# Performance work log

Measured on AMD Instinct MI355X. Metric: run time of the kernel, lower is better.

The kernel has to match this reference:

```python
import jax, jax.numpy as jnp
import numpy as np

B, D, L, K = 4096, 2048, 16384, 64  # batch, input_dim, latent_dim, topk


def setup_inputs() -> dict:
    key = jax.random.key(0)
    k_x, k_w = jax.random.split(key, 2)
    x = jax.random.normal(k_x, (B, D), dtype=jnp.float32)
    # torch init: randn(input_dim, latent_dim) / sqrt(input_dim)
    W_enc = jax.random.normal(k_w, (D, L), dtype=jnp.float32) / np.float32(np.sqrt(D))
    b_enc = jnp.zeros((L,), dtype=jnp.float32)
    b_dec = jnp.zeros((D,), dtype=jnp.float32)
    return {"x": x, "W_enc": W_enc, "b_enc": b_enc, "b_dec": b_dec, "k": K}


def reference(x, W_enc, b_enc, b_dec, k):
    # encode: [B, D] @ [D, L] + [L]
    z = x @ W_enc + b_enc
    # topk sparsify on |z| (do_abs_topk=True): scatter a 0/1 mask, multiply
    _, idx = jax.lax.top_k(jnp.abs(z), k)                      # idx: [B, k]
    rows = jnp.arange(z.shape[0])[:, None]                     # [B, 1]
    mask = jnp.zeros_like(z).at[rows, idx].set(1.0)            # [B, L]
    z_sparse = z * mask
    # decode with tied weights: [B, L] @ [L, D] + [D]
    recon = z_sparse @ W_enc.T + b_dec
    return recon, z_sparse
```

## Files before the change

### kernel.cpp

```cpp
#include <hip/hip_runtime.h>
#include <stdint.h>

#define NB 4096
#define DD 2048
#define LL 16384
#define KT 64
#define WCAP 24
#define TAU 1.2e-2f

typedef unsigned short u16;
typedef __bf16 bf16x8 __attribute__((ext_vector_type(8)));
typedef float f32x4 __attribute__((ext_vector_type(4)));
typedef unsigned short u16x4 __attribute__((ext_vector_type(4)));
typedef unsigned short u16x8 __attribute__((ext_vector_type(8)));

__device__ __forceinline__ float bf2f(u16 b) {
  return __uint_as_float(((unsigned)b) << 16);
}
__device__ __forceinline__ u16 f2bf(float f) {
  unsigned u = __float_as_uint(f);
  unsigned r = u + 0x7fffu + ((u >> 16) & 1u);
  return (u16)(r >> 16);
}

__global__ __launch_bounds__(256) void prep_x(const float* __restrict__ X,
                                              u16* __restrict__ Xh) {
  int i = (blockIdx.x * 256 + threadIdx.x) * 4;
  float4 v = *(const float4*)(X + i);
  u16x4 h;
  h[0] = f2bf(v.x); h[1] = f2bf(v.y); h[2] = f2bf(v.z); h[3] = f2bf(v.w);
  *(u16x4*)(Xh + i) = h;
}

__global__ __launch_bounds__(256) void prep_w(const float* __restrict__ W,
                                              u16* __restrict__ Wh,
                                              float* __restrict__ Wt) {
  __shared__ float tile[64][65];
  int l0 = blockIdx.x * 64, d0 = blockIdx.y * 64;
  int t = threadIdx.x;
  int lx = (t & 15) * 4;
  int dq = t >> 4;
#pragma unroll
  for (int p = 0; p < 4; ++p) {
    int d = dq + p * 16;
    float4 v = *(const float4*)(W + (size_t)(d0 + d) * LL + l0 + lx);
    tile[d][lx + 0] = v.x; tile[d][lx + 1] = v.y;
    tile[d][lx + 2] = v.z; tile[d][lx + 3] = v.w;
  }
  __syncthreads();
  int dx = (t & 15) * 4;
  int lq = t >> 4;
#pragma unroll
  for (int p = 0; p < 4; ++p) {
    int l = lq + p * 16;
    u16x4 h;
    float4 wv;
#pragma unroll
    for (int q = 0; q < 4; ++q) {
      float w = tile[dx + q][l];
      h[q] = f2bf(w);
      ((float*)&wv)[q] = w;
    }
    size_t o = (size_t)(l0 + l) * DD + d0 + dx;
    *(u16x4*)(Wh + o) = h;
    *(float4*)(Wt + o) = wv;
  }
}

#define TBM 256
#define TBN 256
#define TBK 64
#define NKT (DD / TBK)

__device__ __forceinline__ void async16(const u16* g, u16* l) {
  __builtin_amdgcn_global_load_lds(
      (const __attribute__((address_space(1))) unsigned int*)g,
      (__attribute__((address_space(3))) unsigned int*)l, 16, 0, 0);
}

#define STAGE(HF, TAU_)                                                      \
  do {                                                                       \
    const u16* g_ = ((HF) < 2 ? Abase : Bbase) +                             \
                    (size_t)(((HF)&1) * 128 + rr) * DD + ((TAU_) << 6) +     \
                    scol;                                                    \
    u16* l_ = ((HF) < 2 ? As : Bs) + ((TAU_)&1) * (TBM * TBK) +              \
              (((HF)&1) * 128) * TBK + t * 8;                                \
    async16(g_, l_);                                                         \
    async16(g_ + (size_t)64 * DD, l_ + 4096);                                \
  } while (0)

#define LDA(DST, DB, MQ)                                                     \
  do {                                                                       \
    const u16* p_ = As + (DB) * (TBM * TBK) + (wm + (MQ)*64 + fr) * TBK;     \
    _Pragma("unroll") for (int i_ = 0; i_ < 4; ++i_) {                       \
      DST[i_][0] = *(const bf16x8*)(p_ + i_ * (16 * TBK) + c0);              \
      DST[i_][1] = *(const bf16x8*)(p_ + i_ * (16 * TBK) + c1);              \
    }                                                                        \
  } while (0)

#define LDBQ(DB, NQ)                                                         \
  do {                                                                       \
    const u16* p_ = Bs + (DB) * (TBN * TBK) + (wn + (NQ)*32 + fr) * TBK;     \
    _Pragma("unroll") for (int j_ = 0; j_ < 2; ++j_) {                       \
      bq[j_][0] = *(const bf16x8*)(p_ + j_ * (16 * TBK) + c0);               \
      bq[j_][1] = *(const bf16x8*)(p_ + j_ * (16 * TBK) + c1);               \
    }                                                                        \
  } while (0)

#define MFMAQ(AF, MQ, NQ)                                                    \
  do {                                                                       \
    _Pragma("unroll") for (int i_ = 0; i_ < 4; ++i_)                         \
        _Pragma("unroll") for (int j_ = 0; j_ < 2; ++j_) {                   \
      f32x4 a_ = acc[(MQ)*4 + i_][(NQ)*2 + j_];                              \
      a_ = __builtin_amdgcn_mfma_f32_16x16x32_bf16(AF[i_][0], bq[j_][0], a_, \
                                                   0, 0, 0);                 \
      a_ = __builtin_amdgcn_mfma_f32_16x16x32_bf16(AF[i_][1], bq[j_][1], a_, \
                                                   0, 0, 0);                 \
      acc[(MQ)*4 + i_][(NQ)*2 + j_] = a_;                                    \
    }                                                                        \
  } while (0)

#define BAR __builtin_amdgcn_s_barrier()
#define LGKM0 asm volatile("s_waitcnt lgkmcnt(0)")
#define LGKM8 asm volatile("s_waitcnt lgkmcnt(8)")
#define PRIO1 __builtin_amdgcn_s_setprio(1)
#define PRIO0 __builtin_amdgcn_s_setprio(0)

__global__ __launch_bounds__(512, 2) void encode_gemm(
    const u16* __restrict__ Xh,
    const u16* __restrict__ Wh,
    const float* __restrict__ benc,
    float* __restrict__ Z) {
  __shared__ u16 As[2 * TBM * TBK];
  __shared__ u16 Bs[2 * TBN * TBK];
  int t = threadIdx.x;
  int m0 = blockIdx.y * TBM;
  int n0 = blockIdx.x * TBN;

  int lane = t & 63, w = t >> 6;
  int wm = (w & 1) * 128;
  int wn = (w >> 1) * 64;
  int fr = lane & 15;
  int fq = lane >> 4;
  int c0 = ((fq ^ (fr & 7)) << 3);
  int c1 = (((4 + fq) ^ (fr & 7)) << 3);
  int rr = t >> 3;
  int scol = (((t & 7) ^ (rr & 7)) << 3);

  const u16* Abase = Xh + (size_t)m0 * DD;
  const u16* Bbase = Wh + (size_t)n0 * DD;

  f32x4 acc[8][4] = {};
  bf16x8 af0[4][2], af1[4][2], bq[2][2];

  STAGE(0, 0); STAGE(1, 0); STAGE(2, 0); STAGE(3, 0);
  asm volatile("s_waitcnt vmcnt(4)" ::: "memory");
  STAGE(0, 1); STAGE(1, 1); STAGE(2, 1);
  asm volatile("s_waitcnt vmcnt(6)" ::: "memory");
  BAR;

  for (int it = 0; it < NKT / 2; ++it) {
    const int notlast = (it < NKT / 2 - 1);
    LDA(af0, 0, 0);
    LDBQ(0, 0);
    LDA(af1, 0, 1);
    STAGE(3, 2 * it + 1);
    BAR; LGKM8; PRIO1; MFMAQ(af0, 0, 0); PRIO0; BAR;
    LGKM0; PRIO1; MFMAQ(af1, 1, 0); PRIO0;
    LDBQ(0, 1);
    BAR;
    if (notlast) STAGE(0, 2 * it + 2);
    BAR; LGKM0; PRIO1; MFMAQ(af0, 0, 1); PRIO0; BAR;
    if (notlast) { STAGE(1, 2 * it + 2); STAGE(2, 2 * it + 2); }
    BAR; PRIO1; MFMAQ(af1, 1, 1); PRIO0;
    if (notlast) asm volatile("s_waitcnt vmcnt(6)" ::: "memory");
    else         asm volatile("s_waitcnt vmcnt(0)" ::: "memory");
    BAR;
    LDA(af0, 1, 0);
    LDBQ(1, 0);
    LDA(af1, 1, 1);
    if (notlast) STAGE(3, 2 * it + 2);
    BAR; LGKM8; PRIO1; MFMAQ(af0, 0, 0); PRIO0; BAR;
    LGKM0; PRIO1; MFMAQ(af1, 1, 0); PRIO0;
    LDBQ(1, 1);
    BAR;
    if (notlast) STAGE(0, 2 * it + 3);
    BAR; LGKM0; PRIO1; MFMAQ(af0, 0, 1); PRIO0; BAR;
    if (notlast) { STAGE(1, 2 * it + 3); STAGE(2, 2 * it + 3); }
    BAR; PRIO1; MFMAQ(af1, 1, 1); PRIO0;
    if (notlast) asm volatile("s_waitcnt vmcnt(6)" ::: "memory");
    BAR;
  }

  int rbase = m0 + wm + fq * 4;
#pragma unroll
  for (int nr = 0; nr < 4; ++nr) {
    int col = n0 + wn + nr * 16 + fr;
    float be = benc[col];
#pragma unroll
    for (int mr = 0; mr < 8; ++mr) {
      int row = rbase + mr * 16;
#pragma unroll
      for (int r = 0; r < 4; ++r)
        Z[(size_t)(row + r) * LL + col] = acc[mr][nr][r] + be;
    }
  }
}

__global__ __launch_bounds__(512) void topkfix_kernel(
    const float* __restrict__ Z, const float* __restrict__ X32,
    const float* __restrict__ benc, const float* __restrict__ Wt,
    float* __restrict__ ZS, int* __restrict__ TKI, float* __restrict__ TKV,
    int r0) {
  int lrow = blockIdx.x, grow = r0 + lrow, t = threadIdx.x;
  const float* zr = Z + (size_t)lrow * LL;
  float* zs = ZS + (size_t)lrow * LL;

  __shared__ int hist[512];
  __shared__ unsigned cutsh;
  __shared__ int red[2][8];
  __shared__ unsigned nsel, ntie;
  __shared__ int widx[WCAP];

  hist[t & 511] = 0;
  if (t == 0) { cutsh = 0xFFFFFFFFu; nsel = 0; ntie = 0; }
  __syncthreads();

  uint4 kv[8];
#pragma unroll
  for (int i = 0; i < 8; ++i) {
    float4 v = ((const float4*)zr)[t + i * 512];
    kv[i].x = __float_as_uint(v.x) & 0x7fffffffu;
    kv[i].y = __float_as_uint(v.y) & 0x7fffffffu;
    kv[i].z = __float_as_uint(v.z) & 0x7fffffffu;
    kv[i].w = __float_as_uint(v.w) & 0x7fffffffu;
  }
  float4 z4 = {0.f, 0.f, 0.f, 0.f};
#pragma unroll
  for (int i = 0; i < 8; ++i) ((float4*)zs)[t + i * 512] = z4;

  const unsigned thrKey = 0x40000000u;
#pragma unroll
  for (int i = 0; i < 8; ++i) {
    unsigned k4[4] = {kv[i].x, kv[i].y, kv[i].z, kv[i].w};
#pragma unroll
    for (int q = 0; q < 4; ++q) {
      if (k4[q] >= thrKey) {
        int b = (int)((k4[q] >> 16) - 0x4000u);
        if (b > 511) b = 511;
        atomicAdd(&hist[b], 1);
      }
    }
  }
  __syncthreads();

  if (t < 64) {
    int partial[8];
    int s = 0;
    int base_r = t * 8;
#pragma unroll
    for (int q = 0; q < 8; ++q) { partial[q] = hist[511 - (base_r + q)]; s += partial[q]; }
    int sc = s;
#pragma unroll
    for (int off = 1; off < 64; off <<= 1) {
      int up = __shfl_up(sc, off, 64);
      if (t >= off) sc += up;
    }
    int pre = sc - s;
    int total = __shfl(sc, 63, 64);
    if (total >= KT && pre < KT && pre + s >= KT) {
      int run = pre, rstar = -1;
#pragma unroll
      for (int q = 0; q < 8; ++q) {
        run += partial[q];
        if (run >= KT && rstar < 0) rstar = base_r + q;
      }
      int bstar = 511 - rstar;
      cutsh = (bstar == 511) ? 0xFFFFFFFFu
                             : (((unsigned)(0x4000 + bstar)) << 16);
    }
  }
  __syncthreads();

  unsigned cut = cutsh;
  if (cut == 0xFFFFFFFFu) {
    cut = 0;
    for (int bit = 30; bit >= 16; --bit) {
      int ph = bit & 1;
      unsigned ct = cut | (1u << bit);
      int cnt = 0;
#pragma unroll
      for (int i = 0; i < 8; ++i)
        cnt += (kv[i].x >= ct) + (kv[i].y >= ct) + (kv[i].z >= ct) + (kv[i].w >= ct);
      for (int off = 32; off > 0; off >>= 1) cnt += __shfl_down(cnt, off, 64);
      if ((t & 63) == 0) red[ph][t >> 6] = cnt;
      __syncthreads();
      int total = 0;
#pragma unroll
      for (int wv = 0; wv < 8; ++wv) total += red[ph][wv];
      if (total >= KT) cut = ct;
    }
  }

  float c16 = __uint_as_float(cut);
  float cnx = __uint_as_float(cut + 0x10000u);
  float chi = cnx + TAU;
  float clo = c16 - TAU; if (clo < 0.f) clo = 0.f;
  unsigned hiKey = __float_as_uint(chi);
  unsigned loKey = (clo > 0.f) ? __float_as_uint(clo) : 0u;

#pragma unroll
  for (int i = 0; i < 8; ++i) {
    int base = 4 * (t + i * 512);
    unsigned k4[4] = {kv[i].x, kv[i].y, kv[i].z, kv[i].w};
#pragma unroll
    for (int q = 0; q < 4; ++q) {
      unsigned key = k4[q];
      int idx = base + q;
      if (key > hiKey) {
        unsigned p = atomicAdd(&nsel, 1u);
        if (p < KT) {
          float v = zr[idx];
          TKI[grow * KT + p] = idx;
          TKV[grow * KT + p] = v;
          zs[idx] = v;
        }
      } else if (key >= loKey) {
        unsigned p = atomicAdd(&ntie, 1u);
        if (p < WCAP) widx[p] = idx;
      }
    }
  }
  __syncthreads();
  int ns = (int)nsel; if (ns > KT) ns = KT;
  if (t >= ns && t < KT) { TKI[grow * KT + t] = 0; TKV[grow * KT + t] = 0.f; }
  int wcnt = (int)ntie; if (wcnt > WCAP) wcnt = WCAP;
  int deferred = KT - ns;
  if (deferred <= 0) return;
  if (deferred > wcnt) deferred = wcnt;

  if (wcnt == deferred) {
    if (t < wcnt) {
      int idx = widx[t];
      float v = zr[idx];
      TKI[grow * KT + ns + t] = idx;
      TKV[grow * KT + ns + t] = v;
      zs[idx] = v;
    }
    return;
  }

  int wid = t >> 6, ln = t & 63;
  __shared__ float xs[DD];
  __shared__ double wz[WCAP];
  for (int i = t; i < DD; i += 512) xs[i] = X32[(size_t)grow * DD + i];
  __syncthreads();
  for (int j = wid; j < wcnt; j += 8) {
    int idx = widx[j];
    const float* wrow = Wt + (size_t)idx * DD;
    double p = 0.0;
#pragma unroll
    for (int kb = 0; kb < 8; ++kb) {
      int k = kb * 256 + ln * 4;
      f32x4 w4 = *(const f32x4*)(wrow + k);
      f32x4 x4 = *(const f32x4*)(xs + k);
#pragma unroll
      for (int e = 0; e < 4; ++e)
        p += (double)x4[e] * (double)w4[e];
    }
    for (int off = 32; off > 0; off >>= 1) p += __shfl_down(p, off, 64);
    if (ln == 0) wz[j] = p + (double)benc[idx];
  }
  __syncthreads();

  if (t == 0) {
    int taken = 0;
    for (int s = 0; s < deferred; ++s) {
      int best = -1; double bv = -1.0;
      for (int j = 0; j < wcnt; ++j) {
        if (taken & (1 << j)) continue;
        double a = fabs(wz[j]);
        if (best < 0 || a > bv || (a == bv && widx[j] < widx[best])) { best = j; bv = a; }
      }
      taken |= (1 << best);
      int idx = widx[best];
      float v = (float)wz[best];
      TKI[grow * KT + ns + s] = idx;
      TKV[grow * KT + ns + s] = v;
      zs[idx] = v;
    }
  }
}

__global__ __launch_bounds__(256) void decode_kernel(
    const u16* __restrict__ Wh, const float* __restrict__ bdec,
    const int* __restrict__ TKI, const float* __restrict__ TKV,
    float* __restrict__ OUT) {
  int row = blockIdx.x, t = threadIdx.x;
  __shared__ int sidx[KT];
  __shared__ float sval[KT];
  if (t < KT) {
    sidx[t] = TKI[row * KT + t] & (LL - 1);
    sval[t] = TKV[row * KT + t];
  }
  __syncthreads();
  int d0 = t * 8;
  float acc[8] = {0.f, 0.f, 0.f, 0.f, 0.f, 0.f, 0.f, 0.f};
#pragma unroll 16
  for (int j = 0; j < KT; ++j) {
    const u16x8 wv = *(const u16x8*)(Wh + (size_t)sidx[j] * DD + d0);
    float v = sval[j];
#pragma unroll
    for (int e = 0; e < 8; ++e) acc[e] = fmaf(v, bf2f(wv[e]), acc[e]);
  }
  float4 o0, o1;
  o0.x = acc[0] + bdec[d0 + 0]; o0.y = acc[1] + bdec[d0 + 1];
  o0.z = acc[2] + bdec[d0 + 2]; o0.w = acc[3] + bdec[d0 + 3];
  o1.x = acc[4] + bdec[d0 + 4]; o1.y = acc[5] + bdec[d0 + 5];
  o1.z = acc[6] + bdec[d0 + 6]; o1.w = acc[7] + bdec[d0 + 7];
  float* dst = OUT + (size_t)row * DD + d0;
  *(float4*)dst = o0;
  *(float4*)(dst + 4) = o1;
}

extern "C" void kernel_launch(void* const* d_in, const int* in_sizes, int n_in,
                              void* d_out, int out_size, void* d_ws,
                              size_t ws_size, hipStream_t stream) {
  const float* X = (const float*)d_in[0];
  const float* W = (const float*)d_in[1];
  const float* benc = (const float*)d_in[2];
  const float* bdec = (const float*)d_in[3];

  char* ws = (char*)d_ws;
  const size_t XH_B = (size_t)NB * DD * 2;
  const size_t WH_B = (size_t)LL * DD * 2;
  const size_t WT_B = (size_t)LL * DD * 4;
  const size_t TKI_B = (size_t)NB * KT * 4;
  u16* Xh = (u16*)ws;
  u16* Wh = (u16*)(ws + XH_B);
  float* Wt = (float*)(ws + XH_B + WH_B);
  int* TKI = (int*)(ws + XH_B + WH_B + WT_B);
  float* TKV = (float*)(ws + XH_B + WH_B + WT_B + TKI_B);
  float* Zc = (float*)(ws + XH_B + WH_B + WT_B + 2 * TKI_B);

  size_t fixed = XH_B + WH_B + WT_B + 2 * TKI_B;
  size_t avail = (ws_size > fixed) ? (ws_size - fixed) : 0;
  int chunk = (int)(avail / ((size_t)LL * 4));
  chunk = (chunk / TBM) * TBM;
  if (chunk > NB) chunk = NB;
  if (chunk < TBM) chunk = TBM;

  float* out_recon = (float*)d_out;
  float* out_zs = (float*)d_out + (size_t)NB * DD;

  prep_x<<<NB * DD / 1024, 256, 0, stream>>>(X, Xh);
  prep_w<<<dim3(LL / 64, DD / 64), 256, 0, stream>>>(W, Wh, Wt);
  for (int r0 = 0; r0 < NB; r0 += chunk) {
    int rows = NB - r0; if (rows > chunk) rows = chunk;
    encode_gemm<<<dim3(LL / TBN, rows / TBM), 512, 0, stream>>>(
        Xh + (size_t)r0 * DD, Wh, benc, Zc);
    topkfix_kernel<<<rows, 512, 0, stream>>>(
        Zc, X, benc, Wt, out_zs + (size_t)r0 * LL, TKI, TKV, r0);
  }
  decode_kernel<<<NB, 256, 0, stream>>>(Wh, bdec, TKI, TKV, out_recon);
}
```

Before: 1.074 ms.

## Fuse sparse decode into the top-k kernel and drop the decode launch

The separate decode kernel is removed. Each top-k block now keeps its selected indices and values in shared memory and computes its reconstruction row directly, with 512 threads each producing 4 outputs. This avoids writing TKI/TKV to global memory, reading them back, and paying for an extra launch. In exchange the top-k kernel gets longer and uses more registers, which may lower occupancy. The early returns are replaced by barriers that every thread reaches.

```diff
diff --git a/kernel.cpp b/kernel.cpp
--- a/kernel.cpp
+++ b/kernel.cpp
@@ -210,8 +210,8 @@
 __global__ __launch_bounds__(512) void topkfix_kernel(
     const float* __restrict__ Z, const float* __restrict__ X32,
     const float* __restrict__ benc, const float* __restrict__ Wt,
-    float* __restrict__ ZS, int* __restrict__ TKI, float* __restrict__ TKV,
-    int r0) {
+    const u16* __restrict__ Wh, const float* __restrict__ bdec,
+    float* __restrict__ ZS, float* __restrict__ RECON, int r0) {
   int lrow = blockIdx.x, grow = r0 + lrow, t = threadIdx.x;
   const float* zr = Z + (size_t)lrow * LL;
   float* zs = ZS + (size_t)lrow * LL;
@@ -221,6 +221,8 @@
   __shared__ int red[2][8];
   __shared__ unsigned nsel, ntie;
   __shared__ int widx[WCAP];
+  __shared__ int sidx[KT];
+  __shared__ float sval[KT];
 
   hist[t & 511] = 0;
   if (t == 0) { cutsh = 0xFFFFFFFFu; nsel = 0; ntie = 0; }
@@ -321,8 +323,8 @@
         unsigned p = atomicAdd(&nsel, 1u);
         if (p < KT) {
           float v = zr[idx];
-          TKI[grow * KT + p] = idx;
-          TKV[grow * KT + p] = v;
+          sidx[p] = idx;
+          sval[p] = v;
           zs[idx] = v;
         }
       } else if (key >= loKey) {
@@ -333,94 +335,80 @@
   }
   __syncthreads();
   int ns = (int)nsel; if (ns > KT) ns = KT;
-  if (t >= ns && t < KT) { TKI[grow * KT + t] = 0; TKV[grow * KT + t] = 0.f; }
+  if (t >= ns && t < KT) { sidx[t] = 0; sval[t] = 0.f; }
   int wcnt = (int)ntie; if (wcnt > WCAP) wcnt = WCAP;
   int deferred = KT - ns;
-  if (deferred <= 0) return;
   if (deferred > wcnt) deferred = wcnt;
 
-  if (wcnt == deferred) {
-    if (t < wcnt) {
-      int idx = widx[t];
-      float v = zr[idx];
-      TKI[grow * KT + ns + t] = idx;
-      TKV[grow * KT + ns + t] = v;
-      zs[idx] = v;
-    }
-    return;
-  }
-
-  int wid = t >> 6, ln = t & 63;
-  __shared__ float xs[DD];
-  __shared__ double wz[WCAP];
-  for (int i = t; i < DD; i += 512) xs[i] = X32[(size_t)grow * DD + i];
-  __syncthreads();
-  for (int j = wid; j < wcnt; j += 8) {
-    int idx = widx[j];
-    const float* wrow = Wt + (size_t)idx * DD;
-    double p = 0.0;
-#pragma unroll
-    for (int kb = 0; kb < 8; ++kb) {
-      int k = kb * 256 + ln * 4;
-      f32x4 w4 = *(const f32x4*)(wrow + k);
-      f32x4 x4 = *(const f32x4*)(xs + k);
-#pragma unroll
-      for (int e = 0; e < 4; ++e)
-        p += (double)x4[e] * (double)w4[e];
-    }
-    for (int off = 32; off > 0; off >>= 1) p += __shfl_down(p, off, 64);
-    if (ln == 0) wz[j] = p + (double)benc[idx];
-  }
-  __syncthreads();
-
-  if (t == 0) {
-    int taken = 0;
-    for (int s = 0; s < deferred; ++s) {
-      int best = -1; double bv = -1.0;
-      for (int j = 0; j < wcnt; ++j) {
-        if (taken & (1 << j)) continue;
-        double a = fabs(wz[j]);
-        if (best < 0 || a > bv || (a == bv && widx[j] < widx[best])) { best = j; bv = a; }
-      }
-      taken |= (1 << best);
-      int idx = widx[best];
-      float v = (float)wz[best];
-      TKI[grow * KT + ns + s] = idx;
-      TKV[grow * KT + ns + s] = v;
-      zs[idx] = v;
-    }
-  }
-}
-
-__global__ __launch_bounds__(256) void decode_kernel(
-    const u16* __restrict__ Wh, const float* __restrict__ bdec,
-    const int* __restrict__ TKI, const float* __restrict__ TKV,
-    float* __restrict__ OUT) {
-  int row = blockIdx.x, t = threadIdx.x;
-  __shared__ int sidx[KT];
-  __shared__ float sval[KT];
-  if (t < KT) {
-    sidx[t] = TKI[row * KT + t] & (LL - 1);
-    sval[t] = TKV[row * KT + t];
-  }
-  __syncthreads();
-  int d0 = t * 8;
-  float acc[8] = {0.f, 0.f, 0.f, 0.f, 0.f, 0.f, 0.f, 0.f};
-#pragma unroll 16
+  if (deferred > 0) {
+    if (wcnt == deferred) {
+      if (t < wcnt) {
+        int idx = widx[t];
+        float v = zr[idx];
+        sidx[ns + t] = idx;
+        sval[ns + t] = v;
+        zs[idx] = v;
+      }
+    } else {
+      int wid = t >> 6, ln = t & 63;
+      __shared__ float xs[DD];
+      __shared__ double wz[WCAP];
+      for (int i = t; i < DD; i += 512) xs[i] = X32[(size_t)grow * DD + i];
+      __syncthreads();
+      for (int j = wid; j < wcnt; j += 8) {
+        int idx = widx[j];
+        const float* wrow = Wt + (size_t)idx * DD;
+        double p = 0.0;
+#pragma unroll
+        for (int kb = 0; kb < 8; ++kb) {
+          int k = kb * 256 + ln * 4;
+          f32x4 w4 = *(const f32x4*)(wrow + k);
+          f32x4 x4 = *(const f32x4*)(xs + k);
+#pragma unroll
+          for (int e = 0; e < 4; ++e)
+            p += (double)x4[e] * (double)w4[e];
+        }
+        for (int off = 32; off > 0; off >>= 1) p += __shfl_down(p, off, 64);
+        if (ln == 0) wz[j] = p + (double)benc[idx];
+      }
+      __syncthreads();
+
+      if (t == 0) {
+        int taken = 0;
+        for (int s = 0; s < deferred; ++s) {
+          int best = -1; double bv = -1.0;
+          for (int j = 0; j < wcnt; ++j) {
+            if (taken & (1 << j)) continue;
+            double a = fabs(wz[j]);
+            if (best < 0 || a > bv || (a == bv && widx[j] < widx[best])) { best = j; bv = a; }
+          }
+          taken |= (1 << best);
+          int idx = widx[best];
+          float v = (float)wz[best];
+          sidx[ns + s] = idx;
+          sval[ns + s] = v;
+          zs[idx] = v;
+        }
+      }
+    }
+  }
+  __syncthreads();
+
+  int d0 = t * 4;
+  float acc4[4] = {0.f, 0.f, 0.f, 0.f};
+#pragma unroll 8
   for (int j = 0; j < KT; ++j) {
-    const u16x8 wv = *(const u16x8*)(Wh + (size_t)sidx[j] * DD + d0);
+    const u16x4 wv = *(const u16x4*)(Wh + (size_t)sidx[j] * DD + d0);
     float v = sval[j];
 #pragma unroll
-    for (int e = 0; e < 8; ++e) acc[e] = fmaf(v, bf2f(wv[e]), acc[e]);
-  }
-  float4 o0, o1;
-  o0.x = acc[0] + bdec[d0 + 0]; o0.y = acc[1] + bdec[d0 + 1];
-  o0.z = acc[2] + bdec[d0 + 2]; o0.w = acc[3] + bdec[d0 + 3];
-  o1.x = acc[4] + bdec[d0 + 4]; o1.y = acc[5] + bdec[d0 + 5];
-  o1.z = acc[6] + bdec[d0 + 6]; o1.w = acc[7] + bdec[d0 + 7];
-  float* dst = OUT + (size_t)row * DD + d0;
-  *(float4*)dst = o0;
-  *(float4*)(dst + 4) = o1;
+    for (int e = 0; e < 4; ++e) acc4[e] = fmaf(v, bf2f(wv[e]), acc4[e]);
+  }
+  float4 o;
+  o.x = acc4[0] + bdec[d0 + 0];
+  o.y = acc4[1] + bdec[d0 + 1];
+  o.z = acc4[2] + bdec[d0 + 2];
+  o.w = acc4[3] + bdec[d0 + 3];
+  *(float4*)(RECON + (size_t)grow * DD + d0) = o;
 }
 
 extern "C" void kernel_launch(void* const* d_in, const int* in_sizes, int n_in,
@@ -435,15 +423,12 @@
   const size_t XH_B = (size_t)NB * DD * 2;
   const size_t WH_B = (size_t)LL * DD * 2;
   const size_t WT_B = (size_t)LL * DD * 4;
-  const size_t TKI_B = (size_t)NB * KT * 4;
   u16* Xh = (u16*)ws;
   u16* Wh = (u16*)(ws + XH_B);
   float* Wt = (float*)(ws + XH_B + WH_B);
-  int* TKI = (int*)(ws + XH_B + WH_B + WT_B);
-  float* TKV = (float*)(ws + XH_B + WH_B + WT_B + TKI_B);
-  float* Zc = (float*)(ws + XH_B + WH_B + WT_B + 2 * TKI_B);
-
-  size_t fixed = XH_B + WH_B + WT_B + 2 * TKI_B;
+  float* Zc = (float*)(ws + XH_B + WH_B + WT_B);
+
+  size_t fixed = XH_B + WH_B + WT_B;
   size_t avail = (ws_size > fixed) ? (ws_size - fixed) : 0;
   int chunk = (int)(avail / ((size_t)LL * 4));
   chunk = (chunk / TBM) * TBM;
@@ -460,7 +445,6 @@
     encode_gemm<<<dim3(LL / TBN, rows / TBM), 512, 0, stream>>>(
         Xh + (size_t)r0 * DD, Wh, benc, Zc);
     topkfix_kernel<<<rows, 512, 0, stream>>>(
-        Zc, X, benc, Wt, out_zs + (size_t)r0 * LL, TKI, TKV, r0);
-  }
-  decode_kernel<<<NB, 256, 0, stream>>>(Wh, bdec, TKI, TKV, out_recon);
-}
+        Zc, X, benc, Wt, Wh, bdec, out_zs + (size_t)r0 * LL, out_recon, r0);
+  }
+}
```

Measured after the change: 1.021 ms. -5.0%, faster.
